# Optimization experiments

Hardware: AMD Instinct MI355X
Metric: run time of the kernel (lower is better)

## Reference

```python
import jax, jax.numpy as jnp
import numpy as np

MASS = 0.5
G = 1.0  # constant offset -p[8]*g in the objective; does not affect argmin u*
NEWTON_ITERS = 30


def _lambertw(x):
    """Solve w*exp(w) = x for x >= 0 (principal branch) via Newton iterations."""
    w = jnp.log1p(x)  # good init on [0, inf)
    for _ in range(NEWTON_ITERS):
        ew = jnp.exp(w)
        w = w - (w * ew - x) / (ew * (w + 1.0))
    return w


def setup_inputs() -> dict:
    key = jax.random.key(0)
    kz, kt, k1, k2 = jax.random.split(key, 4)
    B, S, H = 500000, 12, 100
    return {
        "z": jax.random.normal(kz, (B, S), jnp.float32),
        "t": jax.random.uniform(kt, (B,), jnp.float32),
        "W1": jax.random.normal(k1, (S + 1, H), jnp.float32) * 0.1,
        "b1": jnp.zeros((H,), jnp.float32),
        "W2": jax.random.normal(k2, (H, S), jnp.float32) * 0.1,
        "b2": jnp.zeros((S,), jnp.float32),
    }


def reference(z, t, W1, b1, W2, b2):
    # p_net: MLP on concat([t, z])
    inp = jnp.concatenate([t[:, None], z], axis=1)          # [B, 13]
    h = jnp.tanh(inp @ W1 + b1)                              # [B, 100]
    p = h @ W2 + b2                                          # [B, 12]
    # Objective: c . u + exp(0.5*||u||^2) + const, with
    # c = [(p6+p7+p8)/m, p9, p10, p11]. Stationarity: c + u*exp(0.5||u||^2)=0
    # => u = -c*exp(-0.5*w), where w = ||u||^2 solves w*e^w = ||c||^2 (Lambert W).
    c = jnp.stack(
        [(p[:, 6] + p[:, 7] + p[:, 8]) / MASS, p[:, 9], p[:, 10], p[:, 11]],
        axis=1,
    )                                                        # [B, 4]
    x = jnp.sum(c * c, axis=1)                               # [B] = ||c||^2
    w = _lambertw(x)                                         # [B]
    ustar = -c * jnp.exp(-0.5 * w)[:, None]                  # [B, 4]
    return ustar
```

## Files before the change

kernel.cpp:

```cpp
#include <hip/hip_runtime.h>


constexpr int S = 12;
constexpr int H = 100;
#define TWO_LOG2E 2.8853900817779268f

typedef float f32x4 __attribute__((ext_vector_type(4)));
typedef __bf16 bf16x8 __attribute__((ext_vector_type(8)));
typedef unsigned int uint4v __attribute__((ext_vector_type(4)));

struct HiLo { unsigned h, l; };

__device__ __forceinline__ float fast_rcp(float x) {
    return __builtin_amdgcn_rcpf(x);
}

__device__ __forceinline__ HiLo split2(float f0, float f1) {
    unsigned b0 = __float_as_uint(f0), b1 = __float_as_uint(f1);
    float h0 = __uint_as_float(b0 & 0xffff0000u);
    float h1 = __uint_as_float(b1 & 0xffff0000u);
    unsigned l0 = __float_as_uint(f0 - h0) >> 16;
    unsigned l1 = __float_as_uint(f1 - h1) >> 16;
    HiLo r;
    r.h = (b0 >> 16) | (b1 & 0xffff0000u);
    r.l = l0 | (l1 << 16);
    return r;
}

__global__ __launch_bounds__(256) void pack_weights(
    const float* __restrict__ W1, const float* __restrict__ b1,
    const float* __restrict__ W2, float* __restrict__ ws)
{
    int idx = blockIdx.x * 256 + threadIdx.x;
    if (idx >= 5632) return;
    unsigned halves[2];
    if (idx < 3584) {
        int d = idx & 3, lane = (idx >> 2) & 63, tp = idx >> 8;
        int t = tp >> 1, p = tp & 1;
        int g = lane >> 4, n = (t << 4) + (lane & 15);
        #pragma unroll
        for (int h = 0; h < 2; ++h) {
            int k = g * 8 + 2 * d + h;
            float f = 0.0f;
            if (n < H) {
                if (k < 13)       f = W1[k * H + n];
                else if (k == 13) f = b1[n];
            }
            unsigned bb = __float_as_uint(f);
            unsigned hb = bb >> 16;
            float hf = __uint_as_float(bb & 0xffff0000u);
            unsigned lb = __float_as_uint(f - hf) >> 16;
            halves[h] = p ? lb : hb;
        }
    } else {
        int r = idx - 3584;
        int d = r & 3, lane = (r >> 2) & 63, sp = r >> 8;
        int s = sp >> 1, p = sp & 1;
        int g = lane >> 4, c = lane & 15;
        #pragma unroll
        for (int h = 0; h < 2; ++h) {
            int k = s * 32 + g * 8 + 2 * d + h;
            float f = (k < H && c < 6) ? W2[k * S + 6 + c] : 0.0f;
            unsigned bb = __float_as_uint(f);
            unsigned hb = bb >> 16;
            float hf = __uint_as_float(bb & 0xffff0000u);
            unsigned lb = __float_as_uint(f - hf) >> 16;
            halves[h] = p ? lb : hb;
        }
    }
    reinterpret_cast<unsigned*>(ws)[idx] = halves[0] | (halves[1] << 16);
}

__global__ __launch_bounds__(256) void cvx_quad_kernel(
    const float* __restrict__ z, const float* __restrict__ t,
    const float* __restrict__ ws, const float* __restrict__ b2,
    float* __restrict__ out, int B, int ntiles, int tpw)
{
    __shared__ float lds[4 * 2240];
    int lane = threadIdx.x & 63;
    int wid  = threadIdx.x >> 6;
    float* wbase = lds + wid * 2240;
    float* pbase = wbase + 16 * 132;
    int g = lane >> 4, c15 = lane & 15;

    int gw = blockIdx.x * 4 + wid;
    int t0 = gw * tpw;
    if (t0 >= ntiles) return;
    int tend = t0 + tpw; if (tend > ntiles) tend = ntiles;

    const uint4v* wsv = reinterpret_cast<const uint4v*>(ws);
    uint4v b1f[7][2], b2f[4][2];
    #pragma unroll
    for (int tt = 0; tt < 7; ++tt) {
        b1f[tt][0] = wsv[(tt * 2 + 0) * 64 + lane];
        b1f[tt][1] = wsv[(tt * 2 + 1) * 64 + lane];
    }
    #pragma unroll
    for (int s = 0; s < 4; ++s) {
        b2f[s][0] = wsv[896 + (s * 2 + 0) * 64 + lane];
        b2f[s][1] = wsv[896 + (s * 2 + 1) * 64 + lane];
    }
    float bb[6];
    #pragma unroll
    for (int c = 0; c < 6; ++c) bb[c] = b2[6 + c];

    {
        int i = lane * 4, m = i >> 4, c = i & 15;
        float4 zz; zz.x = 0.f; zz.y = 0.f; zz.z = 0.f; zz.w = 0.f;
        *reinterpret_cast<float4*>(wbase + m * 132 + 112 + c) = zz;
    }

    auto LOADX = [&](int tile, float xv[8]) {
        int row = tile * 16 + c15; if (row >= B) row = B - 1;
        const float* zr = z + (size_t)row * 12;
        if (g == 0) {
            float4 za = *reinterpret_cast<const float4*>(zr);
            float2 zb = *reinterpret_cast<const float2*>(zr + 4);
            float  zc = zr[6];
            xv[0] = t[row]; xv[1] = za.x; xv[2] = za.y; xv[3] = za.z;
            xv[4] = za.w;   xv[5] = zb.x; xv[6] = zb.y; xv[7] = zc;
        } else if (g == 1) {
            float  zd = zr[7];
            float4 ze = *reinterpret_cast<const float4*>(zr + 8);
            xv[0] = zd;   xv[1] = ze.x; xv[2] = ze.y; xv[3] = ze.z;
            xv[4] = ze.w; xv[5] = 1.0f; xv[6] = 0.0f; xv[7] = 0.0f;
        } else {
            #pragma unroll
            for (int i2 = 0; i2 < 8; ++i2) xv[i2] = 0.0f;
        }
    };

    float xcur[8];
    LOADX(t0, xcur);

    for (int tt = t0; tt < tend; ++tt) {
        uint4v ah, al;
        {
            HiLo r0 = split2(xcur[0], xcur[1]);
            HiLo r1 = split2(xcur[2], xcur[3]);
            HiLo r2 = split2(xcur[4], xcur[5]);
            HiLo r3 = split2(xcur[6], xcur[7]);
            ah.x = r0.h; al.x = r0.l;
            ah.y = r1.h; al.y = r1.l;
            ah.z = r2.h; al.z = r2.l;
            ah.w = r3.h; al.w = r3.l;
        }
        if (tt + 1 < tend) LOADX(tt + 1, xcur);

        bf16x8 A1h = __builtin_bit_cast(bf16x8, ah);
        bf16x8 A1l = __builtin_bit_cast(bf16x8, al);

        #pragma unroll
        for (int nt = 0; nt < 7; ++nt) {
            f32x4 acc = {0.f, 0.f, 0.f, 0.f};
            bf16x8 Bh = __builtin_bit_cast(bf16x8, b1f[nt][0]);
            bf16x8 Bl = __builtin_bit_cast(bf16x8, b1f[nt][1]);
            acc = __builtin_amdgcn_mfma_f32_16x16x32_bf16(A1h, Bh, acc, 0, 0, 0);
            acc = __builtin_amdgcn_mfma_f32_16x16x32_bf16(A1h, Bl, acc, 0, 0, 0);
            acc = __builtin_amdgcn_mfma_f32_16x16x32_bf16(A1l, Bh, acc, 0, 0, 0);
            #pragma unroll
            for (int r = 0; r < 4; ++r) {
                float e  = __builtin_amdgcn_exp2f(acc[r] * TWO_LOG2E);
                float th = fmaf(-2.0f, fast_rcp(e + 1.0f), 1.0f);
                wbase[(g * 4 + r) * 132 + nt * 16 + c15] = th;
            }
        }

        f32x4 p = {0.f, 0.f, 0.f, 0.f};
        #pragma unroll
        for (int s = 0; s < 4; ++s) {
            const float* src = wbase + c15 * 132 + s * 32 + g * 8;
            float4 v0 = *reinterpret_cast<const float4*>(src);
            float4 v1 = *reinterpret_cast<const float4*>(src + 4);
            uint4v a2h, a2l;
            {
                HiLo r0 = split2(v0.x, v0.y);
                HiLo r1 = split2(v0.z, v0.w);
                HiLo r2 = split2(v1.x, v1.y);
                HiLo r3 = split2(v1.z, v1.w);
                a2h.x = r0.h; a2l.x = r0.l;
                a2h.y = r1.h; a2l.y = r1.l;
                a2h.z = r2.h; a2l.z = r2.l;
                a2h.w = r3.h; a2l.w = r3.l;
            }
            bf16x8 A2h = __builtin_bit_cast(bf16x8, a2h);
            bf16x8 A2l = __builtin_bit_cast(bf16x8, a2l);
            bf16x8 Bh = __builtin_bit_cast(bf16x8, b2f[s][0]);
            bf16x8 Bl = __builtin_bit_cast(bf16x8, b2f[s][1]);
            p = __builtin_amdgcn_mfma_f32_16x16x32_bf16(A2h, Bh, p, 0, 0, 0);
            p = __builtin_amdgcn_mfma_f32_16x16x32_bf16(A2h, Bl, p, 0, 0, 0);
            p = __builtin_amdgcn_mfma_f32_16x16x32_bf16(A2l, Bh, p, 0, 0, 0);
        }

        if (c15 < 6) {
            #pragma unroll
            for (int r = 0; r < 4; ++r) pbase[(g * 4 + r) * 8 + c15] = p[r];
        }

        if (lane < 16) {
            int m = lane;
            float4 pa = *reinterpret_cast<const float4*>(pbase + m * 8);
            float2 pb = *reinterpret_cast<const float2*>(pbase + m * 8 + 4);
            float p0 = pa.x + bb[0], p1 = pa.y + bb[1], p2 = pa.z + bb[2];
            float p3 = pa.w + bb[3], p4 = pb.x + bb[4], p5 = pb.y + bb[5];

            float c0 = 2.0f * (p0 + p1 + p2);
            float x = fmaf(c0, c0, fmaf(p3, p3, fmaf(p4, p4, p5 * p5)));

            float w = __logf(1.0f + x);
            #pragma unroll
            for (int it = 0; it < 5; ++it) {
                float ew  = __expf(w);
                float num = fmaf(w, ew, -x);
                float den = fmaf(ew, w, ew);
                w = w - num * fast_rcp(den);
            }
            float sc = -__expf(-0.5f * w);

            int row = tt * 16 + m;
            if (row < B) {
                float4 o;
                o.x = c0 * sc; o.y = p3 * sc; o.z = p4 * sc; o.w = p5 * sc;
                *reinterpret_cast<float4*>(out + (size_t)row * 4) = o;
            }
        }
    }
}

extern "C" void kernel_launch(void* const* d_in, const int* in_sizes, int n_in,
                              void* d_out, int out_size, void* d_ws, size_t ws_size,
                              hipStream_t stream) {
    const float* z  = (const float*)d_in[0];
    const float* t  = (const float*)d_in[1];
    const float* W1 = (const float*)d_in[2];
    const float* b1 = (const float*)d_in[3];
    const float* W2 = (const float*)d_in[4];
    const float* b2 = (const float*)d_in[5];
    float* out = (float*)d_out;
    float* ws  = (float*)d_ws;

    pack_weights<<<dim3(22), dim3(256), 0, stream>>>(W1, b1, W2, ws);

    int B = in_sizes[1];
    int ntiles = (B + 15) / 16;
    int tpw = (ntiles + 3124) / 3125;
    int nwaves = (ntiles + tpw - 1) / tpw;
    int grid = (nwaves + 3) / 4;
    cvx_quad_kernel<<<dim3(grid), dim3(256), 0, stream>>>(
        z, t, ws, b2, out, B, ntiles, tpw);
}
```

Measured before the change: 122.4 us.

## Fuse layer-1 tanh into layer-2 strips, single-bf16 hidden, batch Lambert-W per wave

Layer-1 MFMA output is now consumed in 32-column strips that feed the layer-2 MFMA directly, so the full 16x112 hidden tile is no longer staged in LDS. The 2*log2(e) tanh scale is folded into the packed W1/b1 weights, which removes a multiply per element. The hidden activations go into layer 2 as a single rounded bf16 instead of a hi/lo split, which drops one MFMA per k-step but lowers precision. Each wave now handles 4 tiles and runs the Lambert-W epilogue once over all 64 lanes instead of 16 lanes per tile; this also changes the grid to many more, shorter-lived waves that reload the weights more often.

```diff
diff --git a/kernel.cpp b/kernel.cpp
--- a/kernel.cpp
+++ b/kernel.cpp
@@ -25,6 +25,12 @@
     r.h = (b0 >> 16) | (b1 & 0xffff0000u);
     r.l = l0 | (l1 << 16);
     return r;
+}
+
+__device__ __forceinline__ unsigned pack_rnd(float a, float b) {
+    unsigned ra = __float_as_uint(a) + 0x8000u;
+    unsigned rb = __float_as_uint(b) + 0x8000u;
+    return __builtin_amdgcn_perm(rb, ra, 0x07060302u);
 }
 
 __global__ __launch_bounds__(256) void pack_weights(
@@ -43,8 +49,8 @@
             int k = g * 8 + 2 * d + h;
             float f = 0.0f;
             if (n < H) {
-                if (k < 13)       f = W1[k * H + n];
-                else if (k == 13) f = b1[n];
+                if (k < 13)       f = W1[k * H + n] * TWO_LOG2E;
+                else if (k == 13) f = b1[n] * TWO_LOG2E;
             }
             unsigned bb = __float_as_uint(f);
             unsigned hb = bb >> 16;
@@ -74,19 +80,19 @@
 __global__ __launch_bounds__(256) void cvx_quad_kernel(
     const float* __restrict__ z, const float* __restrict__ t,
     const float* __restrict__ ws, const float* __restrict__ b2,
-    float* __restrict__ out, int B, int ntiles, int tpw)
+    float* __restrict__ out, int B, int ntiles)
 {
-    __shared__ float lds[4 * 2240];
+    __shared__ float lds[4 * 1344];
     int lane = threadIdx.x & 63;
     int wid  = threadIdx.x >> 6;
-    float* wbase = lds + wid * 2240;
-    float* pbase = wbase + 16 * 132;
+    float* strip = lds + wid * 1344;
+    float* pb    = strip + 576;
     int g = lane >> 4, c15 = lane & 15;
 
     int gw = blockIdx.x * 4 + wid;
-    int t0 = gw * tpw;
+    int t0 = gw * 4;
     if (t0 >= ntiles) return;
-    int tend = t0 + tpw; if (tend > ntiles) tend = ntiles;
+    int ntl = ntiles - t0; if (ntl > 4) ntl = 4;
 
     const uint4v* wsv = reinterpret_cast<const uint4v*>(ws);
     uint4v b1f[7][2], b2f[4][2];
@@ -103,12 +109,6 @@
     float bb[6];
     #pragma unroll
     for (int c = 0; c < 6; ++c) bb[c] = b2[6 + c];
-
-    {
-        int i = lane * 4, m = i >> 4, c = i & 15;
-        float4 zz; zz.x = 0.f; zz.y = 0.f; zz.z = 0.f; zz.w = 0.f;
-        *reinterpret_cast<float4*>(wbase + m * 132 + 112 + c) = zz;
-    }
 
     auto LOADX = [&](int tile, float xv[8]) {
         int row = tile * 16 + c15; if (row >= B) row = B - 1;
@@ -133,7 +133,7 @@
     float xcur[8];
     LOADX(t0, xcur);
 
-    for (int tt = t0; tt < tend; ++tt) {
+    for (int q = 0; q < ntl; ++q) {
         uint4v ah, al;
         {
             HiLo r0 = split2(xcur[0], xcur[1]);
@@ -145,64 +145,79 @@
             ah.z = r2.h; al.z = r2.l;
             ah.w = r3.h; al.w = r3.l;
         }
-        if (tt + 1 < tend) LOADX(tt + 1, xcur);
-
+        if (q + 1 < ntl) LOADX(t0 + q + 1, xcur);
         bf16x8 A1h = __builtin_bit_cast(bf16x8, ah);
         bf16x8 A1l = __builtin_bit_cast(bf16x8, al);
-
-        #pragma unroll
-        for (int nt = 0; nt < 7; ++nt) {
-            f32x4 acc = {0.f, 0.f, 0.f, 0.f};
-            bf16x8 Bh = __builtin_bit_cast(bf16x8, b1f[nt][0]);
-            bf16x8 Bl = __builtin_bit_cast(bf16x8, b1f[nt][1]);
-            acc = __builtin_amdgcn_mfma_f32_16x16x32_bf16(A1h, Bh, acc, 0, 0, 0);
-            acc = __builtin_amdgcn_mfma_f32_16x16x32_bf16(A1h, Bl, acc, 0, 0, 0);
-            acc = __builtin_amdgcn_mfma_f32_16x16x32_bf16(A1l, Bh, acc, 0, 0, 0);
-            #pragma unroll
-            for (int r = 0; r < 4; ++r) {
-                float e  = __builtin_amdgcn_exp2f(acc[r] * TWO_LOG2E);
-                float th = fmaf(-2.0f, fast_rcp(e + 1.0f), 1.0f);
-                wbase[(g * 4 + r) * 132 + nt * 16 + c15] = th;
-            }
-        }
 
         f32x4 p = {0.f, 0.f, 0.f, 0.f};
         #pragma unroll
         for (int s = 0; s < 4; ++s) {
-            const float* src = wbase + c15 * 132 + s * 32 + g * 8;
-            float4 v0 = *reinterpret_cast<const float4*>(src);
-            float4 v1 = *reinterpret_cast<const float4*>(src + 4);
-            uint4v a2h, a2l;
+            f32x4 acc0 = {0.f, 0.f, 0.f, 0.f};
             {
-                HiLo r0 = split2(v0.x, v0.y);
-                HiLo r1 = split2(v0.z, v0.w);
-                HiLo r2 = split2(v1.x, v1.y);
-                HiLo r3 = split2(v1.z, v1.w);
-                a2h.x = r0.h; a2l.x = r0.l;
-                a2h.y = r1.h; a2l.y = r1.l;
-                a2h.z = r2.h; a2l.z = r2.l;
-                a2h.w = r3.h; a2l.w = r3.l;
-            }
-            bf16x8 A2h = __builtin_bit_cast(bf16x8, a2h);
-            bf16x8 A2l = __builtin_bit_cast(bf16x8, a2l);
-            bf16x8 Bh = __builtin_bit_cast(bf16x8, b2f[s][0]);
-            bf16x8 Bl = __builtin_bit_cast(bf16x8, b2f[s][1]);
-            p = __builtin_amdgcn_mfma_f32_16x16x32_bf16(A2h, Bh, p, 0, 0, 0);
-            p = __builtin_amdgcn_mfma_f32_16x16x32_bf16(A2h, Bl, p, 0, 0, 0);
-            p = __builtin_amdgcn_mfma_f32_16x16x32_bf16(A2l, Bh, p, 0, 0, 0);
+                bf16x8 Bh = __builtin_bit_cast(bf16x8, b1f[2 * s][0]);
+                bf16x8 Bl = __builtin_bit_cast(bf16x8, b1f[2 * s][1]);
+                acc0 = __builtin_amdgcn_mfma_f32_16x16x32_bf16(A1h, Bh, acc0, 0, 0, 0);
+                acc0 = __builtin_amdgcn_mfma_f32_16x16x32_bf16(A1h, Bl, acc0, 0, 0, 0);
+                acc0 = __builtin_amdgcn_mfma_f32_16x16x32_bf16(A1l, Bh, acc0, 0, 0, 0);
+            }
+            f32x4 acc1 = {0.f, 0.f, 0.f, 0.f};
+            if (s < 3) {
+                bf16x8 Bh = __builtin_bit_cast(bf16x8, b1f[2 * s + 1][0]);
+                bf16x8 Bl = __builtin_bit_cast(bf16x8, b1f[2 * s + 1][1]);
+                acc1 = __builtin_amdgcn_mfma_f32_16x16x32_bf16(A1h, Bh, acc1, 0, 0, 0);
+                acc1 = __builtin_amdgcn_mfma_f32_16x16x32_bf16(A1h, Bl, acc1, 0, 0, 0);
+                acc1 = __builtin_amdgcn_mfma_f32_16x16x32_bf16(A1l, Bh, acc1, 0, 0, 0);
+            }
+
+            #pragma unroll
+            for (int r = 0; r < 4; ++r) {
+                float e  = __builtin_amdgcn_exp2f(acc0[r]);
+                float th = fmaf(-2.0f, fast_rcp(e + 1.0f), 1.0f);
+                strip[(g * 4 + r) * 36 + c15] = th;
+            }
+            if (s < 3) {
+                #pragma unroll
+                for (int r = 0; r < 4; ++r) {
+                    float e  = __builtin_amdgcn_exp2f(acc1[r]);
+                    float th = fmaf(-2.0f, fast_rcp(e + 1.0f), 1.0f);
+                    strip[(g * 4 + r) * 36 + 16 + c15] = th;
+                }
+            }
+
+            uint4v a2;
+            if (s == 3 && g >= 2) {
+                a2.x = 0u; a2.y = 0u; a2.z = 0u; a2.w = 0u;
+            } else {
+                const float* src = strip + c15 * 36 + g * 8;
+                float4 v0 = *reinterpret_cast<const float4*>(src);
+                float4 v1 = *reinterpret_cast<const float4*>(src + 4);
+                a2.x = pack_rnd(v0.x, v0.y);
+                a2.y = pack_rnd(v0.z, v0.w);
+                a2.z = pack_rnd(v1.x, v1.y);
+                a2.w = pack_rnd(v1.z, v1.w);
+            }
+            bf16x8 A2 = __builtin_bit_cast(bf16x8, a2);
+            bf16x8 B2h = __builtin_bit_cast(bf16x8, b2f[s][0]);
+            bf16x8 B2l = __builtin_bit_cast(bf16x8, b2f[s][1]);
+            p = __builtin_amdgcn_mfma_f32_16x16x32_bf16(A2, B2h, p, 0, 0, 0);
+            p = __builtin_amdgcn_mfma_f32_16x16x32_bf16(A2, B2l, p, 0, 0, 0);
         }
 
         if (c15 < 6) {
             #pragma unroll
-            for (int r = 0; r < 4; ++r) pbase[(g * 4 + r) * 8 + c15] = p[r];
-        }
-
-        if (lane < 16) {
-            int m = lane;
-            float4 pa = *reinterpret_cast<const float4*>(pbase + m * 8);
-            float2 pb = *reinterpret_cast<const float2*>(pbase + m * 8 + 4);
+            for (int r = 0; r < 4; ++r)
+                pb[(q * 16 + g * 4 + r) * 12 + c15] = p[r];
+        }
+    }
+
+    if (lane < ntl * 16) {
+        int row = t0 * 16 + lane;
+        if (row < B) {
+            const float* pr = pb + lane * 12;
+            float4 pa = *reinterpret_cast<const float4*>(pr);
+            float2 pv = *reinterpret_cast<const float2*>(pr + 4);
             float p0 = pa.x + bb[0], p1 = pa.y + bb[1], p2 = pa.z + bb[2];
-            float p3 = pa.w + bb[3], p4 = pb.x + bb[4], p5 = pb.y + bb[5];
+            float p3 = pa.w + bb[3], p4 = pv.x + bb[4], p5 = pv.y + bb[5];
 
             float c0 = 2.0f * (p0 + p1 + p2);
             float x = fmaf(c0, c0, fmaf(p3, p3, fmaf(p4, p4, p5 * p5)));
@@ -217,12 +232,9 @@
             }
             float sc = -__expf(-0.5f * w);
 
-            int row = tt * 16 + m;
-            if (row < B) {
-                float4 o;
-                o.x = c0 * sc; o.y = p3 * sc; o.z = p4 * sc; o.w = p5 * sc;
-                *reinterpret_cast<float4*>(out + (size_t)row * 4) = o;
-            }
+            float4 o;
+            o.x = c0 * sc; o.y = p3 * sc; o.z = p4 * sc; o.w = p5 * sc;
+            *reinterpret_cast<float4*>(out + (size_t)row * 4) = o;
         }
     }
 }
@@ -243,9 +255,8 @@
 
     int B = in_sizes[1];
     int ntiles = (B + 15) / 16;
-    int tpw = (ntiles + 3124) / 3125;
-    int nwaves = (ntiles + tpw - 1) / tpw;
+    int nwaves = (ntiles + 3) / 4;
     int grid = (nwaves + 3) / 4;
     cvx_quad_kernel<<<dim3(grid), dim3(256), 0, stream>>>(
-        z, t, ws, b2, out, B, ntiles, tpw);
-}
+        z, t, ws, b2, out, B, ntiles);
+}
```

Result: faster. 104.1 us (-14.9%).
